# Performance work log

Measured on AMD Instinct MI355X. Metric: run time of the kernel, lower is better.

## Reference

```python
import jax, jax.numpy as jnp
import numpy as np

NUM_TOKENS = 8192
CODEBOOK_DIM = 64
BETA = 0.25
DECAY = 0.99
EPS = 1e-05
B, C, H, W = 32, 64, 32, 32


def setup_inputs() -> dict:
    key = jax.random.key(0)
    k1, k2, k3, k4 = jax.random.split(key, 4)
    z = jax.random.normal(k1, (B, C, H, W), dtype=jnp.float32)
    emb = jax.random.normal(k2, (NUM_TOKENS, CODEBOOK_DIM), dtype=jnp.float32)
    ema_w = jax.random.normal(k3, (NUM_TOKENS, CODEBOOK_DIM), dtype=jnp.float32)
    cluster_size = jax.random.uniform(k4, (NUM_TOKENS,), dtype=jnp.float32)
    return {"z": z, "emb": emb, "ema_w": ema_w, "cluster_size": cluster_size}


def reference(z, emb, ema_w, cluster_size):
    # NCHW -> NHWC, flatten to [N, D]
    z_nhwc = jnp.transpose(z, (0, 2, 3, 1))
    z_flat = z_nhwc.reshape(-1, CODEBOOK_DIM)  # [N, D]

    # squared distances: ||z||^2 + ||e||^2 - 2 z e^T  -> [N, K]
    d = (jnp.sum(z_flat * z_flat, axis=1, keepdims=True)
         + jnp.sum(emb * emb, axis=1)
         - 2.0 * jnp.einsum('nd,kd->nk', z_flat, emb))
    idx = jnp.argmin(d, axis=1)  # [N] int

    z_q = emb[idx].reshape(z_nhwc.shape)  # gather + reshape

    # EMA updates (training-mode buffer math); one-hot matmuls expressed as segment sums
    new_cluster = jax.ops.segment_sum(jnp.ones_like(idx, dtype=z.dtype), idx, num_segments=NUM_TOKENS)
    cs = DECAY * cluster_size + (1.0 - DECAY) * new_cluster
    new_ema_w = jax.ops.segment_sum(z_flat, idx, num_segments=NUM_TOKENS)
    ema_w_out = DECAY * ema_w + (1.0 - DECAY) * new_ema_w
    cs_sum = jnp.sum(cs)
    cs_norm = (cs + EPS) / (cs_sum + NUM_TOKENS * EPS)
    emb_out = ema_w_out / cs_norm[:, None]

    # commitment loss uses z_q from the OLD codebook (as in torch code)
    loss = BETA * jnp.mean((jax.lax.stop_gradient(z_q) - z_nhwc) ** 2)

    # straight-through estimator, back to NCHW
    z_q_st = z_nhwc + jax.lax.stop_gradient(z_q - z_nhwc)
    z_q_st = jnp.transpose(z_q_st, (0, 3, 1, 2))
    return z_q_st, loss, idx, cs_norm, ema_w_out, emb_out
```

## Files before the change

### kernel.cpp

```cpp
#include <hip/hip_runtime.h>
#include <float.h>

#define N_TOK   32768
#define DIM     64
#define K_CODES 8192
#define HWSZ    1024
#define CHW     65536
#define NELEM   2097152

typedef short  bf16x8 __attribute__((ext_vector_type(8)));
typedef float  f32x16 __attribute__((ext_vector_type(16)));

static __device__ __forceinline__ unsigned short f2bf(float x) {
    unsigned u = __float_as_uint(x);
    unsigned r = u + 0x7FFFu + ((u >> 16) & 1u);
    return (unsigned short)(r >> 16);
}
static __device__ __forceinline__ float bf2f(unsigned short h) {
    return __uint_as_float(((unsigned)h) << 16);
}

__global__ __launch_bounds__(256) void prep_e(const float* __restrict__ emb,
                                              unsigned short* __restrict__ blob,
                                              float* __restrict__ eng,
                                              unsigned long long* __restrict__ packed,
                                              int* __restrict__ cnt_i,
                                              float* __restrict__ sums) {
    __shared__ float part[512];
    const int gid = blockIdx.x * 256 + threadIdx.x;
    packed[gid] = ~0ull;
    if (gid < K_CODES) cnt_i[gid] = 0;
    if (gid < 2) sums[gid] = 0.f;

    int tile = blockIdx.x;
    #pragma unroll
    for (int u0 = 0; u0 < 2; ++u0) {
        int u = threadIdx.x + u0 * 256;
        int s = u >> 7, h = (u >> 6) & 1, n = u & 63;
        const float* src = emb + (tile * 64 + n) * 64 + s * 16 + h * 8;
        float4 v0 = *(const float4*)src;
        float4 v1 = *(const float4*)(src + 4);
        float x[8] = {v0.x, v0.y, v0.z, v0.w, v1.x, v1.y, v1.z, v1.w};
        unsigned short hi[8], lo[8];
        float ss = 0.f;
        #pragma unroll
        for (int j = 0; j < 8; ++j) {
            hi[j] = f2bf(x[j]);
            lo[j] = f2bf(x[j] - bf2f(hi[j]));
            ss += x[j] * x[j];
        }
        part[u] = ss;
        unsigned short* dhi = blob + (size_t)tile * 8192 + ((s * 2 + 0) * 2 + h) * 512 + n * 8;
        unsigned short* dlo = blob + (size_t)tile * 8192 + ((s * 2 + 1) * 2 + h) * 512 + n * 8;
        uint4 ph, pl;
        ph.x = (unsigned)hi[0] | ((unsigned)hi[1] << 16);
        ph.y = (unsigned)hi[2] | ((unsigned)hi[3] << 16);
        ph.z = (unsigned)hi[4] | ((unsigned)hi[5] << 16);
        ph.w = (unsigned)hi[6] | ((unsigned)hi[7] << 16);
        pl.x = (unsigned)lo[0] | ((unsigned)lo[1] << 16);
        pl.y = (unsigned)lo[2] | ((unsigned)lo[3] << 16);
        pl.z = (unsigned)lo[4] | ((unsigned)lo[5] << 16);
        pl.w = (unsigned)lo[6] | ((unsigned)lo[7] << 16);
        *(uint4*)dhi = ph;
        *(uint4*)dlo = pl;
    }
    __syncthreads();
    if (threadIdx.x < 64) {
        float s = 0.f;
        #pragma unroll
        for (int j = 0; j < 8; ++j) s += part[threadIdx.x + j * 64];
        eng[tile * 64 + threadIdx.x] = s;
    }
}

__global__ __launch_bounds__(256, 3) void vq_argmin(const float* __restrict__ z,
                                                    const unsigned short* __restrict__ blob,
                                                    const float* __restrict__ eng,
                                                    unsigned long long* __restrict__ packed) {
    __shared__ __align__(16) unsigned short zh[64 * 72];
    __shared__ __align__(16) unsigned short zl[64 * 72];
    __shared__ unsigned long long red[64 * 4];

    const int tid  = threadIdx.x;
    const int lane = tid & 63;
    const int wid  = tid >> 6;
    const int l31  = lane & 31, h = lane >> 5;

    const int tb = blockIdx.x & 511;
    const int ks = blockIdx.x >> 9;
    const int n0 = tb * 64;
    const int zbase = (n0 >> 10) * CHW + (n0 & 1023);

    {
        int f4 = tid & 15;
        int c0 = tid >> 4;
        #pragma unroll
        for (int r = 0; r < 4; ++r) {
            int c = c0 * 4 + r;
            float4 v = *(const float4*)(z + zbase + c * HWSZ + f4 * 4);
            float x[4] = {v.x, v.y, v.z, v.w};
            #pragma unroll
            for (int e = 0; e < 4; ++e) {
                int t = f4 * 4 + e;
                float xs = -2.0f * x[e];
                unsigned short hi = f2bf(xs);
                zh[t * 72 + c] = hi;
                zl[t * 72 + c] = f2bf(xs - bf2f(hi));
            }
        }
    }
    __syncthreads();

    bf16x8 T0h[4], T0l[4], T1h[4], T1l[4];
    {
        int r0 = l31;
        int r1 = 32 + l31;
        #pragma unroll
        for (int s = 0; s < 4; ++s) {
            T0h[s] = *(const bf16x8*)(&zh[r0 * 72 + s * 16 + h * 8]);
            T0l[s] = *(const bf16x8*)(&zl[r0 * 72 + s * 16 + h * 8]);
            T1h[s] = *(const bf16x8*)(&zh[r1 * 72 + s * 16 + h * 8]);
            T1l[s] = *(const bf16x8*)(&zl[r1 * 72 + s * 16 + h * 8]);
        }
    }

    const int hk0 = ks * 128 + wid;
    const unsigned short* bp = blob + (size_t)(hk0 >> 1) * 8192 + ((hk0 & 1) * 32 + l31) * 8;
    const float* ep = eng + (hk0 >> 1) * 64 + (hk0 & 1) * 32 + 4 * h;
    int scode = __builtin_amdgcn_readfirstlane((hk0 >> 1) * 64 + (hk0 & 1) * 32);

    bf16x8 Eh[4], El[4];
    #pragma unroll
    for (int s = 0; s < 4; ++s) {
        Eh[s] = *(const bf16x8*)(bp + (4 * s + h) * 512);
        El[s] = *(const bf16x8*)(bp + (4 * s + 2 + h) * 512);
    }
    float4 g0 = *(const float4*)(ep);
    float4 g1 = *(const float4*)(ep + 8);
    float4 g2 = *(const float4*)(ep + 16);
    float4 g3 = *(const float4*)(ep + 24);

    float minv0 = FLT_MAX, minv1 = FLT_MAX;
    int   mini0 = 0,       mini1 = 0;

    for (int i = 0; i < 32; ++i) {
        f32x16 ac0, ac1;
        ac0[0]  = g0.x; ac0[1]  = g0.y; ac0[2]  = g0.z; ac0[3]  = g0.w;
        ac0[4]  = g1.x; ac0[5]  = g1.y; ac0[6]  = g1.z; ac0[7]  = g1.w;
        ac0[8]  = g2.x; ac0[9]  = g2.y; ac0[10] = g2.z; ac0[11] = g2.w;
        ac0[12] = g3.x; ac0[13] = g3.y; ac0[14] = g3.z; ac0[15] = g3.w;
        ac1 = ac0;

        ep += 128;
        g0 = *(const float4*)(ep);
        g1 = *(const float4*)(ep + 8);
        g2 = *(const float4*)(ep + 16);
        g3 = *(const float4*)(ep + 24);

        __builtin_amdgcn_s_setprio(1);
        #pragma unroll
        for (int s = 0; s < 4; ++s) {
            ac0 = __builtin_amdgcn_mfma_f32_32x32x16_bf16(El[s], T0h[s], ac0, 0, 0, 0);
            ac1 = __builtin_amdgcn_mfma_f32_32x32x16_bf16(El[s], T1h[s], ac1, 0, 0, 0);
            ac0 = __builtin_amdgcn_mfma_f32_32x32x16_bf16(Eh[s], T0l[s], ac0, 0, 0, 0);
            ac1 = __builtin_amdgcn_mfma_f32_32x32x16_bf16(Eh[s], T1l[s], ac1, 0, 0, 0);
            ac0 = __builtin_amdgcn_mfma_f32_32x32x16_bf16(Eh[s], T0h[s], ac0, 0, 0, 0);
            ac1 = __builtin_amdgcn_mfma_f32_32x32x16_bf16(Eh[s], T1h[s], ac1, 0, 0, 0);
        }
        __builtin_amdgcn_s_setprio(0);

        bp += 2 * 8192;
        #pragma unroll
        for (int s = 0; s < 4; ++s) {
            Eh[s] = *(const bf16x8*)(bp + (4 * s + h) * 512);
            El[s] = *(const bf16x8*)(bp + (4 * s + 2 + h) * 512);
        }

        #pragma unroll
        for (int r = 0; r < 16; ++r) {
            int code = scode + ((r & 3) + 8 * (r >> 2));
            if (ac0[r] < minv0) { minv0 = ac0[r]; mini0 = code; }
            if (ac1[r] < minv1) { minv1 = ac1[r]; mini1 = code; }
        }
        scode += 128;
    }
    mini0 += 4 * h;
    mini1 += 4 * h;

    unsigned u0 = __float_as_uint(minv0);
    u0 = (u0 & 0x80000000u) ? ~u0 : (u0 | 0x80000000u);
    unsigned long long k0 = ((unsigned long long)u0 << 32) | (unsigned)mini0;
    unsigned u1 = __float_as_uint(minv1);
    u1 = (u1 & 0x80000000u) ? ~u1 : (u1 | 0x80000000u);
    unsigned long long k1 = ((unsigned long long)u1 << 32) | (unsigned)mini1;
    unsigned long long o0 = __shfl_xor(k0, 32, 64);
    if (o0 < k0) k0 = o0;
    unsigned long long o1 = __shfl_xor(k1, 32, 64);
    if (o1 < k1) k1 = o1;
    if (h == 0) {
        red[l31 * 4 + wid]        = k0;
        red[(32 + l31) * 4 + wid] = k1;
    }
    __syncthreads();
    if (tid < 64) {
        unsigned long long a = red[tid * 4], b = red[tid * 4 + 1];
        unsigned long long c = red[tid * 4 + 2], d = red[tid * 4 + 3];
        unsigned long long m = (b < a) ? b : a;
        if (c < m) m = c;
        if (d < m) m = d;
        atomicMin(&packed[n0 + tid], m);
    }
}

__global__ __launch_bounds__(256) void zq_loss(const float* __restrict__ z,
                                               const float* __restrict__ emb,
                                               const float* __restrict__ ema_w,
                                               const unsigned long long* __restrict__ packed,
                                               float* __restrict__ zq_out,
                                               float* __restrict__ idx_out,
                                               int* __restrict__ idx_i32,
                                               int* __restrict__ cnt_i,
                                               float* __restrict__ loss_sum,
                                               float* __restrict__ z_t,
                                               float* __restrict__ emao_out) {
    const int tid = threadIdx.x;
    const int n0  = blockIdx.x * 64;
    const int t   = tid >> 2, q = tid & 3;
    const int n   = n0 + t;
    const int idx = (int)(packed[n] & 0xFFFFFFFFull);
    if (q == 0) {
        idx_out[n] = (float)idx;
        idx_i32[n] = idx;
        atomicAdd(&cnt_i[idx], 1);
    }
    {
        int g = blockIdx.x * 256 + tid;
        #pragma unroll
        for (int j = 0; j < 4; ++j) {
            int i = g + j * 131072;
            emao_out[i] = 0.99f * ema_w[i];
        }
    }
    const int b = n >> 10, hw = n & 1023;
    const float* er = emb + idx * 64 + q * 16;
    float4 e0 = *(const float4*)er, e1 = *(const float4*)(er + 4);
    float4 e2 = *(const float4*)(er + 8), e3 = *(const float4*)(er + 12);
    float ev[16] = {e0.x, e0.y, e0.z, e0.w, e1.x, e1.y, e1.z, e1.w,
                    e2.x, e2.y, e2.z, e2.w, e3.x, e3.y, e3.z, e3.w};
    float lsum = 0.f;
    #pragma unroll
    for (int j = 0; j < 16; ++j) {
        int c = q * 16 + j;
        float zv = z[b * CHW + c * HWSZ + hw];
        float dd = ev[j] - zv;
        zq_out[b * CHW + c * HWSZ + hw] = zv + dd;
        if (z_t) z_t[n * 64 + c] = zv;
        lsum += dd * dd;
    }
    #pragma unroll
    for (int m = 32; m >= 1; m >>= 1) lsum += __shfl_xor(lsum, m, 64);
    if ((tid & 63) == 0) atomicAdd(loss_sum, lsum);
}

__global__ __launch_bounds__(1024) void scan_cs(const int* __restrict__ cnt_i,
                                                const float* __restrict__ csize,
                                                const float* __restrict__ loss_sum,
                                                int* __restrict__ cursor,
                                                float* __restrict__ csn_out,
                                                float* __restrict__ loss_out) {
    __shared__ int   sc[1024];
    __shared__ float sf[1024];
    const int tid = threadIdx.x;
    int v[8], part = 0;
    float cv[8], fpart = 0.f;
    #pragma unroll
    for (int j = 0; j < 8; ++j) { v[j] = cnt_i[tid * 8 + j]; part += v[j]; }
    #pragma unroll
    for (int j = 0; j < 8; ++j) {
        cv[j] = 0.99f * csize[tid * 8 + j] + 0.01f * (float)v[j];
        fpart += cv[j];
    }
    sc[tid] = part;
    sf[tid] = fpart;
    __syncthreads();
    for (int off = 1; off < 1024; off <<= 1) {
        int add = (tid >= off) ? sc[tid - off] : 0;
        __syncthreads();
        sc[tid] += add;
        __syncthreads();
    }
    int run = sc[tid] - part;
    #pragma unroll
    for (int j = 0; j < 8; ++j) {
        cursor[tid * 8 + j] = run;
        run += v[j];
    }
    for (int off = 512; off >= 1; off >>= 1) {
        if (tid < off) sf[tid] += sf[tid + off];
        __syncthreads();
    }
    float denom = sf[0] + (float)(K_CODES * 1e-5);
    #pragma unroll
    for (int j = 0; j < 8; ++j) csn_out[tid * 8 + j] = (cv[j] + 1e-5f) / denom;
    if (tid == 0) *loss_out = 0.25f * (*loss_sum) * (1.0f / (float)NELEM);
}

__global__ __launch_bounds__(256) void scatter_kernel(const int* __restrict__ idx_i32,
                                                      int* __restrict__ cursor,
                                                      int* __restrict__ tok_of,
                                                      int* __restrict__ code_of) {
    int t = blockIdx.x * 256 + threadIdx.x;
    int k = idx_i32[t];
    int pos = atomicAdd(&cursor[k], 1);
    tok_of[pos] = t;
    code_of[pos] = k;
}

__global__ __launch_bounds__(256) void ema_acc(const float* __restrict__ z,
                                               const float* __restrict__ z_t,
                                               const int* __restrict__ tok_of,
                                               const int* __restrict__ code_of,
                                               float* __restrict__ emao_out) {
    const int wv   = (blockIdx.x * 256 + threadIdx.x) >> 6;
    const int lane = threadIdx.x & 63;
    const int pos0 = wv * 64;
    const int tok  = tok_of[pos0 + lane];
    const int cod  = code_of[pos0 + lane];
    float acc = 0.f;
    #pragma unroll
    for (int g = 0; g < 8; ++g) {
        int tk[8], kk[8];
        #pragma unroll
        for (int j = 0; j < 8; ++j) {
            tk[j] = __shfl(tok, g * 8 + j, 64);
            kk[j] = __shfl(cod, g * 8 + j, 64);
        }
        float v[8];
        if (z_t) {
            #pragma unroll
            for (int j = 0; j < 8; ++j) v[j] = z_t[tk[j] * 64 + lane];
        } else {
            #pragma unroll
            for (int j = 0; j < 8; ++j)
                v[j] = z[(tk[j] >> 10) * CHW + lane * HWSZ + (tk[j] & 1023)];
        }
        int knext = (g < 7) ? __shfl(cod, g * 8 + 8, 64) : -1;
        #pragma unroll
        for (int j = 0; j < 8; ++j) {
            acc += v[j];
            int kn = (j < 7) ? kk[j + 1] : knext;
            if (kn != kk[j]) {
                atomicAdd(&emao_out[kk[j] * 64 + lane], 0.01f * acc);
                acc = 0.f;
            }
        }
    }
}

__global__ __launch_bounds__(256) void final_div(const float* __restrict__ emao_out,
                                                 const float* __restrict__ csn_out,
                                                 float* __restrict__ embo_out) {
    int g = blockIdx.x * 256 + threadIdx.x;
    embo_out[g] = emao_out[g] / csn_out[g >> 6];
}

extern "C" void kernel_launch(void* const* d_in, const int* in_sizes, int n_in,
                              void* d_out, int out_size, void* d_ws, size_t ws_size,
                              hipStream_t stream) {
    (void)in_sizes; (void)n_in; (void)out_size;
    const float* z     = (const float*)d_in[0];
    const float* emb   = (const float*)d_in[1];
    const float* ema_w = (const float*)d_in[2];
    const float* csize = (const float*)d_in[3];

    float* out      = (float*)d_out;
    float* zq_out   = out;
    float* loss_out = out + 2097152;
    float* idx_out  = out + 2097153;
    float* csn_out  = out + 2129921;
    float* emao_out = out + 2138113;
    float* embo_out = out + 2662401;

    char* wsb = (char*)d_ws;
    unsigned short*     blob    = (unsigned short*)(wsb);
    float*              eng     = (float*)(wsb + 2097152);
    unsigned long long* packed  = (unsigned long long*)(wsb + 2129920);
    int*                code_of = (int*)(wsb + 2129920);
    int*                idx_i32 = (int*)(wsb + 2392064);
    int*                cnt_i   = (int*)(wsb + 2523136);
    float*              sums    = (float*)(wsb + 2555904);
    int*                cursor  = (int*)(wsb + 2555920);
    int*                tok_of  = (int*)(wsb + 2588688);
    const size_t zt_off = 2719760;
    float* z_t = (ws_size >= zt_off + (size_t)NELEM * 4) ? (float*)(wsb + zt_off) : nullptr;

    prep_e<<<128, 256, 0, stream>>>(emb, blob, eng, packed, cnt_i, sums);
    vq_argmin<<<1024, 256, 0, stream>>>(z, blob, eng, packed);
    zq_loss<<<N_TOK / 64, 256, 0, stream>>>(z, emb, ema_w, packed, zq_out, idx_out,
                                            idx_i32, cnt_i, sums + 1, z_t, emao_out);
    scan_cs<<<1, 1024, 0, stream>>>(cnt_i, csize, sums + 1, cursor, csn_out, loss_out);
    scatter_kernel<<<N_TOK / 256, 256, 0, stream>>>(idx_i32, cursor, tok_of, code_of);
    ema_acc<<<128, 256, 0, stream>>>(z, z_t, tok_of, code_of, emao_out);
    final_div<<<K_CODES * DIM / 256, 256, 0, stream>>>(emao_out, csn_out, embo_out);
}
```

Before: 224.0 us.

## Fuse scan/scatter into zq kernel via last-block and final divide via grid barrier

```diff
diff --git a/kernel.cpp b/kernel.cpp
--- a/kernel.cpp
+++ b/kernel.cpp
@@ -25,12 +25,14 @@
                                               float* __restrict__ eng,
                                               unsigned long long* __restrict__ packed,
                                               int* __restrict__ cnt_i,
-                                              float* __restrict__ sums) {
+                                              float* __restrict__ sums,
+                                              int* __restrict__ ctrs) {
     __shared__ float part[512];
     const int gid = blockIdx.x * 256 + threadIdx.x;
     packed[gid] = ~0ull;
     if (gid < K_CODES) cnt_i[gid] = 0;
     if (gid < 2) sums[gid] = 0.f;
+    if (gid < 2) ctrs[gid] = 0;
 
     int tile = blockIdx.x;
     #pragma unroll
@@ -212,17 +214,28 @@
     }
 }
 
-__global__ __launch_bounds__(256) void zq_loss(const float* __restrict__ z,
-                                               const float* __restrict__ emb,
-                                               const float* __restrict__ ema_w,
-                                               const unsigned long long* __restrict__ packed,
-                                               float* __restrict__ zq_out,
-                                               float* __restrict__ idx_out,
-                                               int* __restrict__ idx_i32,
-                                               int* __restrict__ cnt_i,
-                                               float* __restrict__ loss_sum,
-                                               float* __restrict__ z_t,
-                                               float* __restrict__ emao_out) {
+__global__ __launch_bounds__(256) void zq_fused(const float* __restrict__ z,
+                                                const float* __restrict__ emb,
+                                                const float* __restrict__ ema_w,
+                                                const float* __restrict__ csize,
+                                                const unsigned long long* __restrict__ packed,
+                                                float* __restrict__ zq_out,
+                                                float* __restrict__ idx_out,
+                                                int* __restrict__ idx_i32,
+                                                int* __restrict__ cnt_i,
+                                                float* __restrict__ loss_sum,
+                                                float* __restrict__ z_t,
+                                                float* __restrict__ emao_out,
+                                                int* __restrict__ done_ctr,
+                                                int* __restrict__ tok_of,
+                                                int* __restrict__ code_of,
+                                                float* __restrict__ csn_out,
+                                                float* __restrict__ loss_out) {
+    __shared__ int   curs[8192];
+    __shared__ int   sc[256];
+    __shared__ float sfr[256];
+    __shared__ int   is_last;
+
     const int tid = threadIdx.x;
     const int n0  = blockIdx.x * 64;
     const int t   = tid >> 2, q = tid & 3;
@@ -260,67 +273,64 @@
     #pragma unroll
     for (int m = 32; m >= 1; m >>= 1) lsum += __shfl_xor(lsum, m, 64);
     if ((tid & 63) == 0) atomicAdd(loss_sum, lsum);
-}
-
-__global__ __launch_bounds__(1024) void scan_cs(const int* __restrict__ cnt_i,
-                                                const float* __restrict__ csize,
-                                                const float* __restrict__ loss_sum,
-                                                int* __restrict__ cursor,
-                                                float* __restrict__ csn_out,
-                                                float* __restrict__ loss_out) {
-    __shared__ int   sc[1024];
-    __shared__ float sf[1024];
-    const int tid = threadIdx.x;
-    int v[8], part = 0;
-    float cv[8], fpart = 0.f;
-    #pragma unroll
-    for (int j = 0; j < 8; ++j) { v[j] = cnt_i[tid * 8 + j]; part += v[j]; }
-    #pragma unroll
-    for (int j = 0; j < 8; ++j) {
-        cv[j] = 0.99f * csize[tid * 8 + j] + 0.01f * (float)v[j];
-        fpart += cv[j];
-    }
-    sc[tid] = part;
-    sf[tid] = fpart;
-    __syncthreads();
-    for (int off = 1; off < 1024; off <<= 1) {
+
+    __threadfence();
+    __syncthreads();
+    if (tid == 0) is_last = (atomicAdd(done_ctr, 1) == (int)gridDim.x - 1);
+    __syncthreads();
+    if (!is_last) return;
+    __threadfence();
+
+    int part = 0; float fpart = 0.f;
+    for (int j = 0; j < 32; ++j) {
+        int c = tid * 32 + j;
+        int cnt = cnt_i[c];
+        part  += cnt;
+        fpart += 0.99f * csize[c] + 0.01f * (float)cnt;
+    }
+    sc[tid]  = part;
+    sfr[tid] = fpart;
+    __syncthreads();
+    for (int off = 1; off < 256; off <<= 1) {
         int add = (tid >= off) ? sc[tid - off] : 0;
         __syncthreads();
         sc[tid] += add;
         __syncthreads();
     }
+    for (int off = 128; off >= 1; off >>= 1) {
+        if (tid < off) sfr[tid] += sfr[tid + off];
+        __syncthreads();
+    }
+    float denom = sfr[0] + (float)(K_CODES * 1e-5);
     int run = sc[tid] - part;
-    #pragma unroll
-    for (int j = 0; j < 8; ++j) {
-        cursor[tid * 8 + j] = run;
-        run += v[j];
-    }
-    for (int off = 512; off >= 1; off >>= 1) {
-        if (tid < off) sf[tid] += sf[tid + off];
-        __syncthreads();
-    }
-    float denom = sf[0] + (float)(K_CODES * 1e-5);
-    #pragma unroll
-    for (int j = 0; j < 8; ++j) csn_out[tid * 8 + j] = (cv[j] + 1e-5f) / denom;
+    for (int j = 0; j < 32; ++j) {
+        int c = tid * 32 + j;
+        int cnt = cnt_i[c];
+        float cv = 0.99f * csize[c] + 0.01f * (float)cnt;
+        curs[c] = run;
+        run += cnt;
+        csn_out[c] = (cv + 1e-5f) / denom;
+    }
     if (tid == 0) *loss_out = 0.25f * (*loss_sum) * (1.0f / (float)NELEM);
-}
-
-__global__ __launch_bounds__(256) void scatter_kernel(const int* __restrict__ idx_i32,
-                                                      int* __restrict__ cursor,
-                                                      int* __restrict__ tok_of,
-                                                      int* __restrict__ code_of) {
-    int t = blockIdx.x * 256 + threadIdx.x;
-    int k = idx_i32[t];
-    int pos = atomicAdd(&cursor[k], 1);
-    tok_of[pos] = t;
-    code_of[pos] = k;
-}
-
-__global__ __launch_bounds__(256) void ema_acc(const float* __restrict__ z,
-                                               const float* __restrict__ z_t,
-                                               const int* __restrict__ tok_of,
-                                               const int* __restrict__ code_of,
-                                               float* __restrict__ emao_out) {
+    __syncthreads();
+
+    for (int j = 0; j < 128; ++j) {
+        int tk = j * 256 + tid;
+        int k  = idx_i32[tk];
+        int pos = atomicAdd(&curs[k], 1);
+        tok_of[pos]  = tk;
+        code_of[pos] = k;
+    }
+}
+
+__global__ __launch_bounds__(256) void ema_fused(const float* __restrict__ z,
+                                                 const float* __restrict__ z_t,
+                                                 const int* __restrict__ tok_of,
+                                                 const int* __restrict__ code_of,
+                                                 float* __restrict__ emao_out,
+                                                 const float* __restrict__ csn_out,
+                                                 float* __restrict__ embo_out,
+                                                 int* __restrict__ bar) {
     const int wv   = (blockIdx.x * 256 + threadIdx.x) >> 6;
     const int lane = threadIdx.x & 63;
     const int pos0 = wv * 64;
@@ -355,13 +365,24 @@
             }
         }
     }
-}
-
-__global__ __launch_bounds__(256) void final_div(const float* __restrict__ emao_out,
-                                                 const float* __restrict__ csn_out,
-                                                 float* __restrict__ embo_out) {
-    int g = blockIdx.x * 256 + threadIdx.x;
-    embo_out[g] = emao_out[g] / csn_out[g >> 6];
+
+    __threadfence();
+    __syncthreads();
+    if (threadIdx.x == 0) {
+        atomicAdd(bar, 1);
+        while (atomicAdd(bar, 0) < (int)gridDim.x) __builtin_amdgcn_s_sleep(8);
+    }
+    __syncthreads();
+    __threadfence();
+
+    const int base = blockIdx.x * 4096 + threadIdx.x;
+    #pragma unroll
+    for (int j = 0; j < 16; ++j) {
+        int g = base + j * 256;
+        float ev = __hip_atomic_load(&emao_out[g], __ATOMIC_RELAXED,
+                                     __HIP_MEMORY_SCOPE_AGENT);
+        embo_out[g] = ev / csn_out[g >> 6];
+    }
 }
 
 extern "C" void kernel_launch(void* const* d_in, const int* in_sizes, int n_in,
@@ -389,17 +410,17 @@
     int*                idx_i32 = (int*)(wsb + 2392064);
     int*                cnt_i   = (int*)(wsb + 2523136);
     float*              sums    = (float*)(wsb + 2555904);
-    int*                cursor  = (int*)(wsb + 2555920);
+    int*                ctrs    = (int*)(wsb + 2555920);
     int*                tok_of  = (int*)(wsb + 2588688);
     const size_t zt_off = 2719760;
     float* z_t = (ws_size >= zt_off + (size_t)NELEM * 4) ? (float*)(wsb + zt_off) : nullptr;
 
-    prep_e<<<128, 256, 0, stream>>>(emb, blob, eng, packed, cnt_i, sums);
+    prep_e<<<128, 256, 0, stream>>>(emb, blob, eng, packed, cnt_i, sums, ctrs);
     vq_argmin<<<1024, 256, 0, stream>>>(z, blob, eng, packed);
-    zq_loss<<<N_TOK / 64, 256, 0, stream>>>(z, emb, ema_w, packed, zq_out, idx_out,
-                                            idx_i32, cnt_i, sums + 1, z_t, emao_out);
-    scan_cs<<<1, 1024, 0, stream>>>(cnt_i, csize, sums + 1, cursor, csn_out, loss_out);
-    scatter_kernel<<<N_TOK / 256, 256, 0, stream>>>(idx_i32, cursor, tok_of, code_of);
-    ema_acc<<<128, 256, 0, stream>>>(z, z_t, tok_of, code_of, emao_out);
-    final_div<<<K_CODES * DIM / 256, 256, 0, stream>>>(emao_out, csn_out, embo_out);
-}
+    zq_fused<<<N_TOK / 64, 256, 0, stream>>>(z, emb, ema_w, csize, packed, zq_out,
+                                             idx_out, idx_i32, cnt_i, sums + 1, z_t,
+                                             emao_out, ctrs, tok_of, code_of,
+                                             csn_out, loss_out);
+    ema_fused<<<128, 256, 0, stream>>>(z, z_t, tok_of, code_of, emao_out,
+                                       csn_out, embo_out, ctrs + 1);
+}
```

Measured after the change: 339.2 us. 1.51x slower.

## Stage zq_loss through LDS for coalesced I/O and fuse scatter into scan

Applied to the files above, without the earlier changes.

```diff
diff --git a/kernel.cpp b/kernel.cpp
--- a/kernel.cpp
+++ b/kernel.cpp
@@ -223,10 +223,17 @@
                                                float* __restrict__ loss_sum,
                                                float* __restrict__ z_t,
                                                float* __restrict__ emao_out) {
+    __shared__ float e_lds[64][68];
+    __shared__ float z_lds[64][68];
+
     const int tid = threadIdx.x;
     const int n0  = blockIdx.x * 64;
     const int t   = tid >> 2, q = tid & 3;
     const int n   = n0 + t;
+    const int b   = n0 >> 10;
+    const int hw0 = n0 & 1023;
+    const int zb  = b * CHW + hw0;
+
     const int idx = (int)(packed[n] & 0xFFFFFFFFull);
     if (q == 0) {
         idx_out[n] = (float)idx;
@@ -241,20 +248,52 @@
             emao_out[i] = 0.99f * ema_w[i];
         }
     }
-    const int b = n >> 10, hw = n & 1023;
-    const float* er = emb + idx * 64 + q * 16;
-    float4 e0 = *(const float4*)er, e1 = *(const float4*)(er + 4);
-    float4 e2 = *(const float4*)(er + 8), e3 = *(const float4*)(er + 12);
-    float ev[16] = {e0.x, e0.y, e0.z, e0.w, e1.x, e1.y, e1.z, e1.w,
-                    e2.x, e2.y, e2.z, e2.w, e3.x, e3.y, e3.z, e3.w};
+    {
+        const float* er = emb + idx * 64 + q * 16;
+        float4 e0 = *(const float4*)er,       e1 = *(const float4*)(er + 4);
+        float4 e2 = *(const float4*)(er + 8), e3 = *(const float4*)(er + 12);
+        *(float4*)&e_lds[t][q * 16]      = e0;
+        *(float4*)&e_lds[t][q * 16 + 4]  = e1;
+        *(float4*)&e_lds[t][q * 16 + 8]  = e2;
+        *(float4*)&e_lds[t][q * 16 + 12] = e3;
+    }
+    {
+        const int f4 = tid & 15, c0 = tid >> 4;
+        #pragma unroll
+        for (int r = 0; r < 4; ++r) {
+            int c = c0 * 4 + r;
+            float4 v = *(const float4*)(z + zb + c * HWSZ + f4 * 4);
+            z_lds[f4 * 4 + 0][c] = v.x;
+            z_lds[f4 * 4 + 1][c] = v.y;
+            z_lds[f4 * 4 + 2][c] = v.z;
+            z_lds[f4 * 4 + 3][c] = v.w;
+        }
+    }
+    __syncthreads();
+
+    if (z_t) {
+        #pragma unroll
+        for (int u = 0; u < 4; ++u)
+            *(float4*)&z_t[n * 64 + q * 16 + u * 4] = *(float4*)&z_lds[t][q * 16 + u * 4];
+    }
+    {
+        const int f4 = tid & 15, c0 = tid >> 4;
+        #pragma unroll
+        for (int r = 0; r < 4; ++r) {
+            int c = c0 * 4 + r;
+            float4 o;
+            { float zv = z_lds[f4*4+0][c]; o.x = zv + (e_lds[f4*4+0][c] - zv); }
+            { float zv = z_lds[f4*4+1][c]; o.y = zv + (e_lds[f4*4+1][c] - zv); }
+            { float zv = z_lds[f4*4+2][c]; o.z = zv + (e_lds[f4*4+2][c] - zv); }
+            { float zv = z_lds[f4*4+3][c]; o.w = zv + (e_lds[f4*4+3][c] - zv); }
+            *(float4*)(zq_out + zb + c * HWSZ + f4 * 4) = o;
+        }
+    }
     float lsum = 0.f;
     #pragma unroll
     for (int j = 0; j < 16; ++j) {
         int c = q * 16 + j;
-        float zv = z[b * CHW + c * HWSZ + hw];
-        float dd = ev[j] - zv;
-        zq_out[b * CHW + c * HWSZ + hw] = zv + dd;
-        if (z_t) z_t[n * 64 + c] = zv;
+        float dd = e_lds[t][c] - z_lds[t][c];
         lsum += dd * dd;
     }
     #pragma unroll
@@ -262,14 +301,17 @@
     if ((tid & 63) == 0) atomicAdd(loss_sum, lsum);
 }
 
-__global__ __launch_bounds__(1024) void scan_cs(const int* __restrict__ cnt_i,
-                                                const float* __restrict__ csize,
-                                                const float* __restrict__ loss_sum,
-                                                int* __restrict__ cursor,
-                                                float* __restrict__ csn_out,
-                                                float* __restrict__ loss_out) {
+__global__ __launch_bounds__(1024) void scan_scatter(const int* __restrict__ cnt_i,
+                                                     const float* __restrict__ csize,
+                                                     const float* __restrict__ loss_sum,
+                                                     const int* __restrict__ idx_i32,
+                                                     int* __restrict__ tok_of,
+                                                     int* __restrict__ code_of,
+                                                     float* __restrict__ csn_out,
+                                                     float* __restrict__ loss_out) {
     __shared__ int   sc[1024];
     __shared__ float sf[1024];
+    __shared__ int   curs[8192];
     const int tid = threadIdx.x;
     int v[8], part = 0;
     float cv[8], fpart = 0.f;
@@ -292,7 +334,7 @@
     int run = sc[tid] - part;
     #pragma unroll
     for (int j = 0; j < 8; ++j) {
-        cursor[tid * 8 + j] = run;
+        curs[tid * 8 + j] = run;
         run += v[j];
     }
     for (int off = 512; off >= 1; off >>= 1) {
@@ -303,17 +345,15 @@
     #pragma unroll
     for (int j = 0; j < 8; ++j) csn_out[tid * 8 + j] = (cv[j] + 1e-5f) / denom;
     if (tid == 0) *loss_out = 0.25f * (*loss_sum) * (1.0f / (float)NELEM);
-}
-
-__global__ __launch_bounds__(256) void scatter_kernel(const int* __restrict__ idx_i32,
-                                                      int* __restrict__ cursor,
-                                                      int* __restrict__ tok_of,
-                                                      int* __restrict__ code_of) {
-    int t = blockIdx.x * 256 + threadIdx.x;
-    int k = idx_i32[t];
-    int pos = atomicAdd(&cursor[k], 1);
-    tok_of[pos] = t;
-    code_of[pos] = k;
+    __syncthreads();
+
+    for (int j = 0; j < 32; ++j) {
+        int tk = j * 1024 + tid;
+        int k  = idx_i32[tk];
+        int pos = atomicAdd(&curs[k], 1);
+        tok_of[pos]  = tk;
+        code_of[pos] = k;
+    }
 }
 
 __global__ __launch_bounds__(256) void ema_acc(const float* __restrict__ z,
@@ -389,7 +429,6 @@
     int*                idx_i32 = (int*)(wsb + 2392064);
     int*                cnt_i   = (int*)(wsb + 2523136);
     float*              sums    = (float*)(wsb + 2555904);
-    int*                cursor  = (int*)(wsb + 2555920);
     int*                tok_of  = (int*)(wsb + 2588688);
     const size_t zt_off = 2719760;
     float* z_t = (ws_size >= zt_off + (size_t)NELEM * 4) ? (float*)(wsb + zt_off) : nullptr;
@@ -398,8 +437,8 @@
     vq_argmin<<<1024, 256, 0, stream>>>(z, blob, eng, packed);
     zq_loss<<<N_TOK / 64, 256, 0, stream>>>(z, emb, ema_w, packed, zq_out, idx_out,
                                             idx_i32, cnt_i, sums + 1, z_t, emao_out);
-    scan_cs<<<1, 1024, 0, stream>>>(cnt_i, csize, sums + 1, cursor, csn_out, loss_out);
-    scatter_kernel<<<N_TOK / 256, 256, 0, stream>>>(idx_i32, cursor, tok_of, code_of);
+    scan_scatter<<<1, 1024, 0, stream>>>(cnt_i, csize, sums + 1, idx_i32,
+                                         tok_of, code_of, csn_out, loss_out);
     ema_acc<<<128, 256, 0, stream>>>(z, z_t, tok_of, code_of, emao_out);
     final_div<<<K_CODES * DIM / 256, 256, 0, stream>>>(emao_out, csn_out, embo_out);
 }
```

Result: slower. 260.0 us (+16.1%).
